# Kernel optimization log

Hardware: AMD Instinct MI355X
Metric: run time of the kernel (lower is better)

The kernel has to match this reference:

```python
import jax, jax.numpy as jnp
import numpy as np

B, T, F, H, V = 4096, 128, 256, 64, 32
EMB = 8
IN = EMB + 1  # 8-dim feature embedding + 1 Y_past channel
EPS = 1e-3    # keras LayerNorm/BatchNorm default epsilon


def lstm(x, Wk, Wr, b, h0, c0):
    """Keras-convention LSTM (gate order i,f,g,o). x: [B,T,D] -> ([B,T,H], h, c)."""
    def step(carry, xt):
        h, c = carry
        z = xt @ Wk + h @ Wr + b
        i, f, g, o = jnp.split(z, 4, axis=-1)
        c = jax.nn.sigmoid(f) * c + jax.nn.sigmoid(i) * jnp.tanh(g)
        h = jax.nn.sigmoid(o) * jnp.tanh(c)
        return (h, c), h
    (h, c), hs = jax.lax.scan(step, (h0, c0), jnp.swapaxes(x, 0, 1))
    return jnp.swapaxes(hs, 0, 1), h, c


def setup_inputs() -> dict:
    key = jax.random.key(0)
    ks = iter(jax.random.split(key, 32))
    n = lambda *s: jax.random.normal(next(ks), s, jnp.float32) * 0.05
    return {
        "X": jax.random.normal(next(ks), (B, T, F), jnp.float32),
        "Y_past": jax.random.randint(next(ks), (B, T), 0, V),
        "ln_gamma": jnp.ones((F,), jnp.float32), "ln_beta": jnp.zeros((F,), jnp.float32),
        "W1": n(F, 32), "b1": jnp.zeros((32,), jnp.float32),
        "bn_gamma": jnp.ones((32,), jnp.float32), "bn_beta": jnp.zeros((32,), jnp.float32),
        "bn_mean": jnp.zeros((32,), jnp.float32), "bn_var": jnp.ones((32,), jnp.float32),
        "W2": n(32, 16), "b2": jnp.zeros((16,), jnp.float32),
        "W3": n(16, EMB), "b3": jnp.zeros((EMB,), jnp.float32),
        "enc_fk": n(IN, 4 * H), "enc_fr": n(H, 4 * H), "enc_fb": jnp.zeros((4 * H,), jnp.float32),
        "enc_bk": n(IN, 4 * H), "enc_br": n(H, 4 * H), "enc_bb": jnp.zeros((4 * H,), jnp.float32),
        "Wsh": n(2 * H, H), "bsh": jnp.zeros((H,), jnp.float32),
        "Wsc": n(2 * H, H), "bsc": jnp.zeros((H,), jnp.float32),
        "Wq": n(H, 2 * H), "bq": jnp.zeros((2 * H,), jnp.float32),
        "dec_k": n(2 * H, 4 * H), "dec_r": n(H, 4 * H), "dec_b": jnp.zeros((4 * H,), jnp.float32),
        "Wo": n(H, V), "bo": jnp.zeros((V,), jnp.float32),
    }


def reference(X, Y_past, ln_gamma, ln_beta, W1, b1, bn_gamma, bn_beta, bn_mean, bn_var,
              W2, b2, W3, b3, enc_fk, enc_fr, enc_fb, enc_bk, enc_br, enc_bb,
              Wsh, bsh, Wsc, bsc, Wq, bq, dec_k, dec_r, dec_b, Wo, bo):
    b = X.shape[0]
    # LayerNorm over feature axis
    mu = jnp.mean(X, axis=-1, keepdims=True)
    var = jnp.var(X, axis=-1, keepdims=True)
    xn = (X - mu) * jax.lax.rsqrt(var + EPS) * ln_gamma + ln_beta
    # feature MLP (dropout inactive at inference); BatchNorm in inference mode
    e = jax.nn.relu(xn @ W1 + b1)
    e = (e - bn_mean) * jax.lax.rsqrt(bn_var + EPS) * bn_gamma + bn_beta
    e = jax.nn.relu(e @ W2 + b2)
    e = jax.nn.relu(e @ W3 + b3)
    seq = jnp.concatenate([e, Y_past.astype(jnp.float32)[..., None]], axis=-1)  # [B,T,9]
    # Bidirectional LSTM encoder (merge_mode='concat')
    h0 = jnp.zeros((b, H), seq.dtype)
    c0 = jnp.zeros((b, H), seq.dtype)
    fwd_out, fh, fc = lstm(seq, enc_fk, enc_fr, enc_fb, h0, c0)
    bwd_out, bh, bc = lstm(seq[:, ::-1], enc_bk, enc_br, enc_bb, h0, c0)
    enc = jnp.concatenate([fwd_out, bwd_out[:, ::-1]], axis=-1)  # [B,T,2H]
    # state projections and query
    sh = jnp.concatenate([fh, bh], axis=-1) @ Wsh + bsh  # [B,H]
    sc = jnp.concatenate([fc, bc], axis=-1) @ Wsc + bsc  # [B,H]
    q = (sh @ Wq + bq)[:, None, :]                       # [B,1,2H]
    # keras Attention: dot-product scores, softmax over keys
    scores = jnp.einsum('bqd,btd->bqt', q, enc)
    w = jax.nn.softmax(scores, axis=-1)
    att = jnp.einsum('bqt,btd->bqd', w, enc)             # [B,1,2H]
    # decoder LSTM (length-1 sequence) with projected initial state
    dec_out, _, _ = lstm(att, dec_k, dec_r, dec_b, sh, sc)  # [B,1,H]
    return jax.nn.softmax(dec_out @ Wo + bo, axis=-1)       # [B,1,V]
```

## Files before the change

### kernel.cpp

```cpp
#include <hip/hip_runtime.h>
#include <math.h>

#define BB 4096
#define TT 128
#define FF 256
#define VV 32
#define LN_EPS 1e-3f

typedef __attribute__((ext_vector_type(8))) short short8;
typedef __attribute__((ext_vector_type(4))) float f32x4;

template <int M> struct IC { static constexpr int value = M; };

__device__ __forceinline__ float sigm(float x) {
    return __builtin_amdgcn_rcpf(1.0f + __builtin_amdgcn_exp2f(-1.442695041f * x));
}
__device__ __forceinline__ float tanhfast(float x) {
    float e = __builtin_amdgcn_exp2f(2.885390082f * x);
    return 1.0f - 2.0f * __builtin_amdgcn_rcpf(e + 1.0f);
}
__device__ __forceinline__ unsigned short f2bf(float f) {
    union { float f; unsigned u; } v; v.f = f;
    unsigned r = v.u + 0x7FFFu + ((v.u >> 16) & 1u);
    return (unsigned short)(r >> 16);
}
__device__ __forceinline__ float bf2f(unsigned short h) {
    union { unsigned u; float f; } v; v.u = ((unsigned)h) << 16; return v.f;
}

__global__ __launch_bounds__(256, 3) void k_mlp2(
    const float* __restrict__ X, const int* __restrict__ Yp,
    const float* __restrict__ lng, const float* __restrict__ lnb,
    const float* __restrict__ W1, const float* __restrict__ b1,
    const float* __restrict__ bng, const float* __restrict__ bnb,
    const float* __restrict__ bnm, const float* __restrict__ bnv,
    const float* __restrict__ W2, const float* __restrict__ b2,
    const float* __restrict__ W3, const float* __restrict__ b3,
    unsigned int* __restrict__ sqpk, unsigned short* __restrict__ yv)
{
    __shared__ unsigned short w1fh[8192], w1fl[8192];
    __shared__ unsigned short w2fh[512], w2fl[512];
    __shared__ unsigned short w3fh[512], w3fl[512];
    __shared__ float bD1[32], bnSs[32], bnBs[32], b2s[16], b3s[8];
    __shared__ float e1s[4][16][33];
    __shared__ float e2s[4][16][17];

    const int tid = threadIdx.x;
    for (int e = tid; e < 8192; e += 256) {
        int j = e & 7, lane = (e >> 3) & 63, nt = (e >> 9) & 1, ks = e >> 10;
        int c = ks * 32 + (lane >> 4) * 8 + j;
        int n = nt * 16 + (lane & 15);
        float v = lng[c] * W1[c * 32 + n];
        unsigned short hi = f2bf(v);
        w1fh[e] = hi; w1fl[e] = f2bf(v - bf2f(hi));
    }
    for (int e = tid; e < 512; e += 256) {
        int j = e & 7, lane = e >> 3;
        int k = (lane >> 4) * 8 + j, n = lane & 15;
        float v2 = W2[k * 16 + n];
        unsigned short h2 = f2bf(v2);
        w2fh[e] = h2; w2fl[e] = f2bf(v2 - bf2f(h2));
        float v3 = (k < 16 && n < 8) ? W3[k * 8 + n] : 0.f;
        unsigned short h3 = f2bf(v3);
        w3fh[e] = h3; w3fl[e] = f2bf(v3 - bf2f(h3));
    }
    if (tid < 32) {
        float a = b1[tid];
        for (int c2 = 0; c2 < 256; ++c2) a += lnb[c2] * W1[c2 * 32 + tid];
        bD1[tid] = a;
        float sc = bng[tid] * rsqrtf(bnv[tid] + LN_EPS);
        bnSs[tid] = sc; bnBs[tid] = bnb[tid] - bnm[tid] * sc;
    } else if (tid < 48) b2s[tid - 32] = b2[tid - 32];
    else if (tid < 56) b3s[tid - 48] = b3[tid - 48];
    __syncthreads();

    const int wv = tid >> 6, l = tid & 63;
    const int r = l & 15, q = l >> 4;
    const int ntiles = (BB * TT) / 16;
    for (int tile = blockIdx.x * 4 + wv; tile < ntiles; tile += gridDim.x * 4) {
        const size_t rowbase = (size_t)tile * 16;
        const float* xrow = X + (rowbase + r) * FF + q * 8;
        float xd[64];
        #pragma unroll
        for (int ks = 0; ks < 8; ++ks) {
            float4 p0 = *(const float4*)(xrow + ks * 32);
            float4 p1 = *(const float4*)(xrow + ks * 32 + 4);
            xd[ks * 8 + 0] = p0.x; xd[ks * 8 + 1] = p0.y; xd[ks * 8 + 2] = p0.z; xd[ks * 8 + 3] = p0.w;
            xd[ks * 8 + 4] = p1.x; xd[ks * 8 + 5] = p1.y; xd[ks * 8 + 6] = p1.z; xd[ks * 8 + 7] = p1.w;
        }
        float s = 0.f, ss = 0.f;
        #pragma unroll
        for (int i = 0; i < 64; ++i) { s += xd[i]; ss += xd[i] * xd[i]; }
        s += __shfl_xor(s, 16);  s += __shfl_xor(s, 32);
        ss += __shfl_xor(ss, 16); ss += __shfl_xor(ss, 32);
        float mu = s * (1.0f / FF);
        float var = ss * (1.0f / FF) - mu * mu;
        float rs = rsqrtf(var + LN_EPS);

        f32x4 acc0 = {bD1[r], bD1[r], bD1[r], bD1[r]};
        f32x4 acc1 = {bD1[16 + r], bD1[16 + r], bD1[16 + r], bD1[16 + r]};
        #pragma unroll
        for (int ks = 0; ks < 8; ++ks) {
            short8 ah, al;
            #pragma unroll
            for (int j = 0; j < 8; ++j) {
                float xn = (xd[ks * 8 + j] - mu) * rs;
                unsigned short hi = f2bf(xn);
                ah[j] = (short)hi; al[j] = (short)f2bf(xn - bf2f(hi));
            }
            short8 bh0 = *(const short8*)&w1fh[((ks * 2 + 0) * 64 + l) * 8];
            short8 bl0 = *(const short8*)&w1fl[((ks * 2 + 0) * 64 + l) * 8];
            short8 bh1 = *(const short8*)&w1fh[((ks * 2 + 1) * 64 + l) * 8];
            short8 bl1 = *(const short8*)&w1fl[((ks * 2 + 1) * 64 + l) * 8];
            acc0 = __builtin_amdgcn_mfma_f32_16x16x32_bf16(ah, bh0, acc0, 0, 0, 0);
            acc0 = __builtin_amdgcn_mfma_f32_16x16x32_bf16(al, bh0, acc0, 0, 0, 0);
            acc0 = __builtin_amdgcn_mfma_f32_16x16x32_bf16(ah, bl0, acc0, 0, 0, 0);
            acc1 = __builtin_amdgcn_mfma_f32_16x16x32_bf16(ah, bh1, acc1, 0, 0, 0);
            acc1 = __builtin_amdgcn_mfma_f32_16x16x32_bf16(al, bh1, acc1, 0, 0, 0);
            acc1 = __builtin_amdgcn_mfma_f32_16x16x32_bf16(ah, bl1, acc1, 0, 0, 0);
        }
        #pragma unroll
        for (int i = 0; i < 4; ++i) {
            int row = q * 4 + i;
            float z0 = fmaxf(acc0[i], 0.f) * bnSs[r] + bnBs[r];
            float z1 = fmaxf(acc1[i], 0.f) * bnSs[16 + r] + bnBs[16 + r];
            e1s[wv][row][r] = z0;
            e1s[wv][row][16 + r] = z1;
        }
        __builtin_amdgcn_wave_barrier();

        short8 a2h, a2l;
        #pragma unroll
        for (int j = 0; j < 8; ++j) {
            float v = e1s[wv][r][q * 8 + j];
            unsigned short hi = f2bf(v);
            a2h[j] = (short)hi; a2l[j] = (short)f2bf(v - bf2f(hi));
        }
        f32x4 acc2 = {b2s[r], b2s[r], b2s[r], b2s[r]};
        {
            short8 bh = *(const short8*)&w2fh[l * 8];
            short8 bl = *(const short8*)&w2fl[l * 8];
            acc2 = __builtin_amdgcn_mfma_f32_16x16x32_bf16(a2h, bh, acc2, 0, 0, 0);
            acc2 = __builtin_amdgcn_mfma_f32_16x16x32_bf16(a2l, bh, acc2, 0, 0, 0);
            acc2 = __builtin_amdgcn_mfma_f32_16x16x32_bf16(a2h, bl, acc2, 0, 0, 0);
        }
        #pragma unroll
        for (int i = 0; i < 4; ++i) e2s[wv][q * 4 + i][r] = fmaxf(acc2[i], 0.f);
        __builtin_amdgcn_wave_barrier();

        short8 a3h = (short8){0,0,0,0,0,0,0,0}, a3l = (short8){0,0,0,0,0,0,0,0};
        if (q < 2) {
            #pragma unroll
            for (int j = 0; j < 8; ++j) {
                float v = e2s[wv][r][q * 8 + j];
                unsigned short hi = f2bf(v);
                a3h[j] = (short)hi; a3l[j] = (short)f2bf(v - bf2f(hi));
            }
        }
        float b3v = (r < 8) ? b3s[r] : 0.f;
        f32x4 acc3 = {b3v, b3v, b3v, b3v};
        {
            short8 bh = *(const short8*)&w3fh[l * 8];
            short8 bl = *(const short8*)&w3fl[l * 8];
            acc3 = __builtin_amdgcn_mfma_f32_16x16x32_bf16(a3h, bh, acc3, 0, 0, 0);
            acc3 = __builtin_amdgcn_mfma_f32_16x16x32_bf16(a3l, bh, acc3, 0, 0, 0);
            acc3 = __builtin_amdgcn_mfma_f32_16x16x32_bf16(a3h, bl, acc3, 0, 0, 0);
        }
        if (r < 8) {
            #pragma unroll
            for (int i = 0; i < 4; ++i) {
                size_t grow = rowbase + q * 4 + i;
                float e3 = fmaxf(acc3[i], 0.f);
                unsigned short bfh = f2bf(e3);
                unsigned short bfe = f2bf(e3 - bf2f(bfh));
                unsigned int wself = ((unsigned)bfh << 16) | (unsigned)bfe;
                unsigned int wnbr = __shfl_xor(wself, 1);
                unsigned int outw = (r & 1) ? ((wself << 16) | (wnbr & 0xFFFFu))
                                            : ((wnbr & 0xFFFF0000u) | (wself >> 16));
                sqpk[grow * 8 + (r >> 1) + ((r & 1) ? 4 : 0)] = outw;
            }
        } else if (r == 8) {
            #pragma unroll
            for (int i = 0; i < 4; ++i) {
                size_t grow = rowbase + q * 4 + i;
                yv[grow] = f2bf((float)Yp[grow]);
            }
        }
        __builtin_amdgcn_wave_barrier();
    }
}

#define R1_SEQ 0u
#define R1_YV  65536u
#define R1_HP  69632u
#define R1_SZ  87040u

__global__ __launch_bounds__(512, 1) void k_rnn1(
    const unsigned int* __restrict__ g_sqpk, const unsigned short* __restrict__ g_yv,
    const float* __restrict__ fk, const float* __restrict__ fr, const float* __restrict__ fb,
    const float* __restrict__ bk, const float* __restrict__ br, const float* __restrict__ bbv,
    unsigned int* __restrict__ enc,
    float* __restrict__ hfin, float* __restrict__ cfin,
    int s0)
{
    __shared__ __align__(16) unsigned char arena[R1_SZ];
    unsigned int*  seqU   = (unsigned int*)(arena + R1_SEQ);
    unsigned short* yvS   = (unsigned short*)(arena + R1_YV);
    unsigned int*  hpackU = (unsigned int*)(arena + R1_HP);

    const int tid = threadIdx.x;
    const int sbase = s0 + blockIdx.x * 16;
    const int wv = tid >> 6, l = tid & 63;
    const int d = wv >> 2, w = wv & 3;
    const int r = l & 15, q = l >> 4;
    const int u = (w << 4) + r;

    for (int i = tid; i < 16 * TT * 8; i += 512) {
        int smp = i >> 10;
        int rem = i & 1023;
        int t = rem >> 3, j = rem & 7;
        unsigned int v = g_sqpk[(size_t)(sbase + smp) * (TT * 8) + rem];
        seqU[((t * 2 + (j >> 2)) * 16 + smp) * 4 + (j & 3)] = v;
    }
    for (int i = tid; i < 16 * TT; i += 512) {
        int smp = i >> 7, t = i & 127;
        yvS[t * 16 + smp] = g_yv[(size_t)(sbase + smp) * TT + t];
    }

    const float* Wr = d ? br : fr;
    const float* Wk = d ? bk : fk;
    const float* Bz = d ? bbv : fb;
    short8 Bh[3][4], Bl[3][4];
    float bz[4];
    #pragma unroll
    for (int g = 0; g < 4; ++g) {
        int col = (g << 6) + u;
        bz[g] = Bz[col];
        #pragma unroll
        for (int kt = 0; kt < 3; ++kt) {
            #pragma unroll
            for (int j = 0; j < 8; ++j) {
                int kg = kt * 32 + q * 8 + j;
                float v = (kg < 64) ? Wr[kg * 256 + col]
                        : (kg < 73) ? Wk[(kg - 64) * 256 + col] : 0.f;
                unsigned short hi = f2bf(v);
                Bh[kt][g][j] = (short)hi;
                Bl[kt][g][j] = (short)f2bf(v - bf2f(hi));
            }
        }
    }

    const unsigned int* hrd0 = hpackU + (d * 16 + r) * 68 + q * 4;
    const unsigned int* hrd1 = hrd0 + 2176;
    const int wofs = w * 8 + (r >> 1) + ((r & 1) ? 32 : 0);
    const int elb = ((blockIdx.x * 16 + q * 4) * TT) * 64 + d * 32 + (u >> 1);

    for (int i = tid; i < 4352; i += 512) hpackU[i] = 0u;
    float c4[4] = {0.f, 0.f, 0.f, 0.f};
    __syncthreads();

    for (int t = 0; t < TT; ++t) {
        const int ts = d ? (TT - 1 - t) : t;
        const int buf = t & 1;
        const unsigned int* hp = buf ? hrd1 : hrd0;
        short8 A0h = *(const short8*)(hp);
        short8 A1h = *(const short8*)(hp + 16);
        short8 A0l = *(const short8*)(hp + 32);
        short8 A1l = *(const short8*)(hp + 48);
        short8 A2h = (short8){0,0,0,0,0,0,0,0};
        short8 A2l = (short8){0,0,0,0,0,0,0,0};
        if (q == 0) {
            const unsigned int* sp = seqU + (ts * 32 + r) * 4;
            A2h = *(const short8*)sp;
            A2l = *(const short8*)(sp + 64);
        } else if (q == 1) {
            A2h[0] = (short)yvS[ts * 16 + r];
        }
        f32x4 z[4];
        #pragma unroll
        for (int g = 0; g < 4; ++g) {
            f32x4 acc = {bz[g], bz[g], bz[g], bz[g]};
            acc = __builtin_amdgcn_mfma_f32_16x16x32_bf16(A0h, Bh[0][g], acc, 0, 0, 0);
            acc = __builtin_amdgcn_mfma_f32_16x16x32_bf16(A0l, Bh[0][g], acc, 0, 0, 0);
            acc = __builtin_amdgcn_mfma_f32_16x16x32_bf16(A0h, Bl[0][g], acc, 0, 0, 0);
            acc = __builtin_amdgcn_mfma_f32_16x16x32_bf16(A1h, Bh[1][g], acc, 0, 0, 0);
            acc = __builtin_amdgcn_mfma_f32_16x16x32_bf16(A1l, Bh[1][g], acc, 0, 0, 0);
            acc = __builtin_amdgcn_mfma_f32_16x16x32_bf16(A1h, Bl[1][g], acc, 0, 0, 0);
            acc = __builtin_amdgcn_mfma_f32_16x16x32_bf16(A2h, Bh[2][g], acc, 0, 0, 0);
            acc = __builtin_amdgcn_mfma_f32_16x16x32_bf16(A2l, Bh[2][g], acc, 0, 0, 0);
            acc = __builtin_amdgcn_mfma_f32_16x16x32_bf16(A2h, Bl[2][g], acc, 0, 0, 0);
            z[g] = acc;
        }
        const int nbase = ((buf ^ 1) * 2 + d) * 16;
        #pragma unroll
        for (int i = 0; i < 4; ++i) {
            float zi = z[0][i], zf = z[1][i], zg = z[2][i], zo = z[3][i];
            float cc = sigm(zf) * c4[i] + sigm(zi) * tanhfast(zg);
            float hh = sigm(zo) * tanhfast(cc);
            c4[i] = cc;
            int smp = (q << 2) + i;
            unsigned short bfh = f2bf(hh);
            unsigned short bfe = f2bf(hh - bf2f(bfh));
            unsigned int wself = ((unsigned)bfh << 16) | (unsigned)bfe;
            unsigned int wnbr = __shfl_xor(wself, 1);
            unsigned int outw = (r & 1) ? ((wself << 16) | (wnbr & 0xFFFFu))
                                        : ((wnbr & 0xFFFF0000u) | (wself >> 16));
            hpackU[(nbase + smp) * 68 + wofs] = outw;
            if ((r & 1) == 0) enc[elb + i * (TT * 64) + ts * 64] = outw;
            if (t == TT - 1) {
                hfin[(size_t)(sbase + smp) * 128 + (d << 6) + u] = hh;
                cfin[(size_t)(sbase + smp) * 128 + (d << 6) + u] = cc;
            }
        }
        __syncthreads();
    }
}

__global__ __launch_bounds__(256, 4) void k_att(
    const unsigned short* __restrict__ enc,
    const float* __restrict__ hfin, const float* __restrict__ cfin,
    const float* __restrict__ Wsh, const float* __restrict__ bsh,
    const float* __restrict__ Wsc, const float* __restrict__ bsc,
    const float* __restrict__ Wq,  const float* __restrict__ bq,
    const float* __restrict__ dk,  const float* __restrict__ dr, const float* __restrict__ dbv,
    const float* __restrict__ Wo,  const float* __restrict__ bo,
    float* __restrict__ out, int s0)
{
    __shared__ unsigned short el[TT][136];
    __shared__ float st[128], ct[128], shS[64], scS[64], qS[128], pS[128], attS[128], zdS[256], hdS[64], red[8];

    int tid = threadIdx.x;
    int bloc = blockIdx.x;
    int s = s0 + bloc;

    for (int i = tid; i < TT * 16; i += 256) {
        int t = i >> 4, c = i & 15;
        *(short8*)&el[t][c * 8] = *(const short8*)&enc[(size_t)bloc * TT * 128 + t * 128 + c * 8];
    }
    if (tid < 128) { st[tid] = hfin[(size_t)s * 128 + tid]; ct[tid] = cfin[(size_t)s * 128 + tid]; }
    __syncthreads();

    if (tid < 128) {
        int uu = tid & 63;
        const float* Wm = (tid < 64) ? Wsh : Wsc;
        const float* sv = (tid < 64) ? st : ct;
        float a = (tid < 64) ? bsh[uu] : bsc[uu];
        #pragma unroll 4
        for (int j = 0; j < 128; ++j) a += sv[j] * Wm[j * 64 + uu];
        if (tid < 64) shS[uu] = a; else scS[uu] = a;
    }
    __syncthreads();
    if (tid < 128) {
        float a = bq[tid];
        #pragma unroll 4
        for (int uu = 0; uu < 64; ++uu) a += shS[uu] * Wq[uu * 128 + tid];
        qS[tid] = a;
    }
    __syncthreads();
    float sc_val = 0.f;
    int wvv = tid >> 6, lnn = tid & 63;
    if (tid < 128) {
        float a = 0.f;
        #pragma unroll 2
        for (int c = 0; c < 16; ++c) {
            short8 e8 = *(const short8*)&el[tid][c * 8];
            #pragma unroll
            for (int j2 = 0; j2 < 8; ++j2) a += qS[c * 8 + j2] * bf2f((unsigned short)e8[j2]);
        }
        sc_val = a;
        float m = a;
        #pragma unroll
        for (int mk = 1; mk < 64; mk <<= 1) m = fmaxf(m, __shfl_xor(m, mk));
        if (lnn == 0) red[wvv] = m;
    }
    __syncthreads();
    float gmax = fmaxf(red[0], red[1]);
    if (tid < 128) {
        float ev = expf(sc_val - gmax);
        pS[tid] = ev;
        float s2 = ev;
        #pragma unroll
        for (int mk = 1; mk < 64; mk <<= 1) s2 += __shfl_xor(s2, mk);
        if (lnn == 0) red[4 + wvv] = s2;
    }
    __syncthreads();
    float denom = red[4] + red[5];
    if (tid < 128) {
        float a = 0.f;
        #pragma unroll 4
        for (int t2 = 0; t2 < TT; ++t2) a += pS[t2] * bf2f(el[t2][tid]);
        attS[tid] = a / denom;
    }
    __syncthreads();
    if (tid < 256) {
        float a = dbv[tid];
        #pragma unroll 4
        for (int j = 0; j < 128; ++j) a += attS[j] * dk[j * 256 + tid];
        #pragma unroll 4
        for (int j = 0; j < 64; ++j)  a += shS[j] * dr[j * 256 + tid];
        zdS[tid] = a;
    }
    __syncthreads();
    if (tid < 64) {
        float zi = zdS[tid], zf = zdS[64 + tid], zg = zdS[128 + tid], zo = zdS[192 + tid];
        float cc = sigm(zf) * scS[tid] + sigm(zi) * tanhfast(zg);
        hdS[tid] = sigm(zo) * tanhfast(cc);
    }
    __syncthreads();
    if (tid < 32) {
        float a = bo[tid];
        #pragma unroll
        for (int uu = 0; uu < 64; ++uu) a += hdS[uu] * Wo[uu * 32 + tid];
        float m = a;
        #pragma unroll
        for (int mk = 1; mk < 32; mk <<= 1) m = fmaxf(m, __shfl_xor(m, mk));
        float e = expf(a - m);
        float s2 = e;
        #pragma unroll
        for (int mk = 1; mk < 32; mk <<= 1) s2 += __shfl_xor(s2, mk);
        out[(size_t)s * VV + tid] = e / s2;
    }
}

#define A_SEQ   0u
#define A_YV    65536u
#define A_HP    69632u
#define A_SGRID 87040u
#define A_SH    103424u
#define A_SC    107520u
#define A_Q     111616u
#define A_ATT   119808u
#define A_L     128000u
#define A_SZ    128064u

__global__ __launch_bounds__(512, 1) void k_rnn(
    const unsigned int* __restrict__ g_sqpk, const unsigned short* __restrict__ g_yv,
    const float* __restrict__ fk, const float* __restrict__ fr, const float* __restrict__ fb,
    const float* __restrict__ bk, const float* __restrict__ br, const float* __restrict__ bbv,
    const float* __restrict__ Wsh, const float* __restrict__ bsh,
    const float* __restrict__ Wsc, const float* __restrict__ bsc,
    const float* __restrict__ Wq,  const float* __restrict__ bq,
    const float* __restrict__ dk,  const float* __restrict__ dr, const float* __restrict__ db,
    const float* __restrict__ Wo,  const float* __restrict__ bo,
    float* __restrict__ out)
{
    __shared__ __align__(16) unsigned char arena[A_SZ];
    unsigned int*  seqU  = (unsigned int*)(arena + A_SEQ);
    unsigned short* yvS  = (unsigned short*)(arena + A_YV);
    unsigned int*  hpackU = (unsigned int*)(arena + A_HP);
    float* sgridF = (float*)(arena + A_SGRID);
    float* hfinL  = (float*)(arena + A_SGRID);
    float* cfinL  = hfinL + 2048;
    float* zdS    = (float*)(arena + A_SGRID);
    float* shS    = (float*)(arena + A_SH);
    float* scS    = (float*)(arena + A_SC);
    float* qS     = (float*)(arena + A_Q);
    float* pT     = (float*)(arena + A_Q);
    float* attS   = (float*)(arena + A_ATT);
    float* hdS    = (float*)(arena + A_ATT);
    float* lS     = (float*)(arena + A_L);

    const int tid = threadIdx.x;
    const int sbase = blockIdx.x * 16;
    const int wv = tid >> 6, l = tid & 63;
    const int d = wv >> 2, w = wv & 3;
    const int r = l & 15, q = l >> 4;
    const int u = (w << 4) + r;

    for (int i = tid; i < 16 * TT * 8; i += 512) {
        int smp = i >> 10;
        int rem = i & 1023;
        int t = rem >> 3, j = rem & 7;
        unsigned int v = g_sqpk[(size_t)(sbase + smp) * (TT * 8) + rem];
        seqU[((t * 2 + (j >> 2)) * 16 + smp) * 4 + (j & 3)] = v;
    }
    for (int i = tid; i < 16 * TT; i += 512) {
        int smp = i >> 7, t = i & 127;
        yvS[t * 16 + smp] = g_yv[(size_t)(sbase + smp) * TT + t];
    }

    const float* Wr = d ? br : fr;
    const float* Wk = d ? bk : fk;
    const float* Bz = d ? bbv : fb;
    short8 Bh[3][4], Bl[3][4];
    float bz[4];
    #pragma unroll
    for (int g = 0; g < 4; ++g) {
        int col = (g << 6) + u;
        bz[g] = Bz[col];
        #pragma unroll
        for (int kt = 0; kt < 3; ++kt) {
            #pragma unroll
            for (int j = 0; j < 8; ++j) {
                int kg = kt * 32 + q * 8 + j;
                float v = (kg < 64) ? Wr[kg * 256 + col]
                        : (kg < 73) ? Wk[(kg - 64) * 256 + col] : 0.f;
                unsigned short hi = f2bf(v);
                Bh[kt][g][j] = (short)hi;
                Bl[kt][g][j] = (short)f2bf(v - bf2f(hi));
            }
        }
    }
    short8 Bq0h = (short8){0,0,0,0,0,0,0,0}, Bq1h = (short8){0,0,0,0,0,0,0,0};

    const unsigned int* hrd0 = hpackU + (d * 16 + r) * 68 + q * 4;
    const unsigned int* hrd1 = hrd0 + 2176;
    const int wofs = w * 8 + (r >> 1) + ((r & 1) ? 32 : 0);
    __syncthreads();

    auto run_phase = [&](auto mode_c) {
        constexpr int mode = decltype(mode_c)::value;
        for (int i = tid; i < 4352; i += 512) hpackU[i] = 0u;
        float c4[4] = {0.f, 0.f, 0.f, 0.f};
        float aacc[4] = {0.f, 0.f, 0.f, 0.f};
        __syncthreads();
        for (int t = 0; t < TT; ++t) {
            const int ts = d ? (TT - 1 - t) : t;
            const int buf = t & 1;
            const unsigned int* hp = buf ? hrd1 : hrd0;
            short8 A0h = *(const short8*)(hp);
            short8 A1h = *(const short8*)(hp + 16);
            short8 A0l = *(const short8*)(hp + 32);
            short8 A1l = *(const short8*)(hp + 48);
            short8 A2h = (short8){0,0,0,0,0,0,0,0};
            short8 A2l = (short8){0,0,0,0,0,0,0,0};
            if (q == 0) {
                const unsigned int* sp = seqU + (ts * 32 + r) * 4;
                A2h = *(const short8*)sp;
                A2l = *(const short8*)(sp + 64);
            } else if (q == 1) {
                A2h[0] = (short)yvS[ts * 16 + r];
            }
            if constexpr (mode == 1) {
                if (w == 0 && t > 0) {
                    f32x4 sa = {0.f, 0.f, 0.f, 0.f};
                    sa = __builtin_amdgcn_mfma_f32_16x16x32_bf16(A0h, Bq0h, sa, 0, 0, 0);
                    sa = __builtin_amdgcn_mfma_f32_16x16x32_bf16(A1h, Bq1h, sa, 0, 0, 0);
                    if (q == (r >> 2)) {
                        int tp = d ? (TT - t) : (t - 1);
                        sgridF[(d * 16 + r) * 128 + tp] = sa[r & 3];
                    }
                }
            }
            f32x4 z[4];
            #pragma unroll
            for (int g = 0; g < 4; ++g) {
                f32x4 acc = {bz[g], bz[g], bz[g], bz[g]};
                acc = __builtin_amdgcn_mfma_f32_16x16x32_bf16(A0h, Bh[0][g], acc, 0, 0, 0);
                acc = __builtin_amdgcn_mfma_f32_16x16x32_bf16(A0l, Bh[0][g], acc, 0, 0, 0);
                acc = __builtin_amdgcn_mfma_f32_16x16x32_bf16(A0h, Bl[0][g], acc, 0, 0, 0);
                acc = __builtin_amdgcn_mfma_f32_16x16x32_bf16(A1h, Bh[1][g], acc, 0, 0, 0);
                acc = __builtin_amdgcn_mfma_f32_16x16x32_bf16(A1l, Bh[1][g], acc, 0, 0, 0);
                acc = __builtin_amdgcn_mfma_f32_16x16x32_bf16(A1h, Bl[1][g], acc, 0, 0, 0);
                acc = __builtin_amdgcn_mfma_f32_16x16x32_bf16(A2h, Bh[2][g], acc, 0, 0, 0);
                acc = __builtin_amdgcn_mfma_f32_16x16x32_bf16(A2l, Bh[2][g], acc, 0, 0, 0);
                acc = __builtin_amdgcn_mfma_f32_16x16x32_bf16(A2h, Bl[2][g], acc, 0, 0, 0);
                z[g] = acc;
            }
            const int nbase = ((buf ^ 1) * 2 + d) * 16;
            #pragma unroll
            for (int i = 0; i < 4; ++i) {
                float zi = z[0][i], zf = z[1][i], zg = z[2][i], zo = z[3][i];
                float cc = sigm(zf) * c4[i] + sigm(zi) * tanhfast(zg);
                float hh = sigm(zo) * tanhfast(cc);
                c4[i] = cc;
                int smp = (q << 2) + i;
                unsigned short bfh = f2bf(hh);
                unsigned short bfe = f2bf(hh - bf2f(bfh));
                unsigned int wself = ((unsigned)bfh << 16) | (unsigned)bfe;
                unsigned int wnbr = __shfl_xor(wself, 1);
                unsigned int outw = (r & 1) ? ((wself << 16) | (wnbr & 0xFFFFu))
                                            : ((wnbr & 0xFFFF0000u) | (wself >> 16));
                hpackU[(nbase + smp) * 68 + wofs] = outw;
                if constexpr (mode == 2) aacc[i] += pT[ts * 16 + smp] * hh;
                if constexpr (mode == 0) {
                    if (t == TT - 1) {
                        hfinL[smp * 128 + (d << 6) + u] = hh;
                        cfinL[smp * 128 + (d << 6) + u] = cc;
                    }
                }
            }
            __syncthreads();
        }
        if constexpr (mode == 1) {
            if (w == 0) {
                short8 A0h = *(const short8*)(hrd0);
                short8 A1h = *(const short8*)(hrd0 + 16);
                f32x4 sa = {0.f, 0.f, 0.f, 0.f};
                sa = __builtin_amdgcn_mfma_f32_16x16x32_bf16(A0h, Bq0h, sa, 0, 0, 0);
                sa = __builtin_amdgcn_mfma_f32_16x16x32_bf16(A1h, Bq1h, sa, 0, 0, 0);
                if (q == (r >> 2)) {
                    int tp = d ? 0 : (TT - 1);
                    sgridF[(d * 16 + r) * 128 + tp] = sa[r & 3];
                }
            }
            __syncthreads();
        }
        if constexpr (mode == 2) {
            #pragma unroll
            for (int i = 0; i < 4; ++i) {
                int smp = (q << 2) + i;
                attS[smp * 128 + (d << 6) + u] = aacc[i] / lS[smp];
            }
            __syncthreads();
        }
    };

    run_phase(IC<0>{});
    for (int o = tid; o < 2048; o += 512) {
        int kind = o >> 10, smp = (o >> 6) & 15, uu = o & 63;
        const float* src = kind ? (cfinL + smp * 128) : (hfinL + smp * 128);
        const float* Wm = kind ? Wsc : Wsh;
        float a = kind ? bsc[uu] : bsh[uu];
        #pragma unroll 4
        for (int j = 0; j < 128; ++j) a += src[j] * Wm[j * 64 + uu];
        (kind ? scS : shS)[smp * 64 + uu] = a;
    }
    __syncthreads();
    for (int o = tid; o < 2048; o += 512) {
        int smp = o >> 7, dd = o & 127;
        float a = bq[dd];
        #pragma unroll 4
        for (int j = 0; j < 64; ++j) a += shS[smp * 64 + j] * Wq[j * 128 + dd];
        qS[smp * 128 + dd] = a;
    }
    __syncthreads();
    if (w == 0) {
        #pragma unroll
        for (int j = 0; j < 8; ++j) {
            Bq0h[j] = (short)f2bf(qS[r * 128 + (d << 6) + q * 8 + j]);
            Bq1h[j] = (short)f2bf(qS[r * 128 + (d << 6) + 32 + q * 8 + j]);
        }
    }
    __syncthreads();

    run_phase(IC<1>{});
    {
        int smp = tid >> 5, sl = tid & 31;
        float sv[4];
        #pragma unroll
        for (int p = 0; p < 4; ++p) {
            int t = sl + 32 * p;
            sv[p] = sgridF[smp * 128 + t] + sgridF[(16 + smp) * 128 + t];
        }
        float m = fmaxf(fmaxf(sv[0], sv[1]), fmaxf(sv[2], sv[3]));
        #pragma unroll
        for (int mk = 1; mk < 32; mk <<= 1) m = fmaxf(m, __shfl_xor(m, mk));
        float lsum = 0.f;
        #pragma unroll
        for (int p = 0; p < 4; ++p) lsum += __expf(sv[p] - m);
        #pragma unroll
        for (int mk = 1; mk < 32; mk <<= 1) lsum += __shfl_xor(lsum, mk);
        __syncthreads();
        #pragma unroll
        for (int p = 0; p < 4; ++p) pT[(sl + 32 * p) * 16 + smp] = __expf(sv[p] - m);
        if (sl == 0) lS[smp] = lsum;
    }
    __syncthreads();

    run_phase(IC<2>{});

    for (int o = tid; o < 4096; o += 512) {
        int smp = o >> 8, col = o & 255;
        float a = db[col];
        #pragma unroll 4
        for (int j = 0; j < 128; ++j) a += attS[smp * 128 + j] * dk[j * 256 + col];
        #pragma unroll 4
        for (int j = 0; j < 64; ++j)  a += shS[smp * 64 + j] * dr[j * 256 + col];
        zdS[smp * 256 + col] = a;
    }
    __syncthreads();
    for (int o = tid; o < 1024; o += 512) {
        int smp = o >> 6, uu = o & 63;
        float zi = zdS[smp * 256 + uu], zf = zdS[smp * 256 + 64 + uu];
        float zg = zdS[smp * 256 + 128 + uu], zo = zdS[smp * 256 + 192 + uu];
        float cc = sigm(zf) * scS[smp * 64 + uu] + sigm(zi) * tanhfast(zg);
        hdS[smp * 64 + uu] = sigm(zo) * tanhfast(cc);
    }
    __syncthreads();
    {
        int smp = tid >> 5, v = tid & 31;
        float a = bo[v];
        #pragma unroll 4
        for (int j = 0; j < 64; ++j) a += hdS[smp * 64 + j] * Wo[j * 32 + v];
        float m = a;
        #pragma unroll
        for (int mk = 1; mk < 32; mk <<= 1) m = fmaxf(m, __shfl_xor(m, mk));
        float e = __expf(a - m);
        float s2 = e;
        #pragma unroll
        for (int mk = 1; mk < 32; mk <<= 1) s2 += __shfl_xor(s2, mk);
        out[(size_t)(sbase + smp) * VV + v] = e / s2;
    }
}

extern "C" void kernel_launch(void* const* d_in, const int* in_sizes, int n_in,
                              void* d_out, int out_size, void* d_ws, size_t ws_size,
                              hipStream_t stream) {
    const float* X   = (const float*)d_in[0];
    const int*   Yp  = (const int*)d_in[1];
    const float* lng = (const float*)d_in[2];
    const float* lnb = (const float*)d_in[3];
    const float* W1  = (const float*)d_in[4];
    const float* b1  = (const float*)d_in[5];
    const float* bng = (const float*)d_in[6];
    const float* bnb = (const float*)d_in[7];
    const float* bnm = (const float*)d_in[8];
    const float* bnv = (const float*)d_in[9];
    const float* W2  = (const float*)d_in[10];
    const float* b2  = (const float*)d_in[11];
    const float* W3  = (const float*)d_in[12];
    const float* b3  = (const float*)d_in[13];
    const float* fk  = (const float*)d_in[14];
    const float* fr  = (const float*)d_in[15];
    const float* fb  = (const float*)d_in[16];
    const float* bk  = (const float*)d_in[17];
    const float* br  = (const float*)d_in[18];
    const float* bbv = (const float*)d_in[19];
    const float* Wsh = (const float*)d_in[20];
    const float* bsh = (const float*)d_in[21];
    const float* Wsc = (const float*)d_in[22];
    const float* bsc = (const float*)d_in[23];
    const float* Wq  = (const float*)d_in[24];
    const float* bq  = (const float*)d_in[25];
    const float* dk  = (const float*)d_in[26];
    const float* dr  = (const float*)d_in[27];
    const float* db  = (const float*)d_in[28];
    const float* Wo  = (const float*)d_in[29];
    const float* bo  = (const float*)d_in[30];

    unsigned int*   sqpk = (unsigned int*)d_ws;
    unsigned short* yv   = (unsigned short*)(sqpk + (size_t)BB * TT * 8);
    float*          hfin = (float*)(yv + (size_t)BB * TT);
    float*          cfin = hfin + (size_t)BB * 128;
    unsigned int*   encp = (unsigned int*)(cfin + (size_t)BB * 128);
    const size_t baseB = (size_t)((char*)encp - (char*)d_ws);

    int nch = 0;
    if (ws_size >= baseB + (size_t)BB * TT * 128 * 2)            nch = 1;
    else if (ws_size >= baseB + (size_t)(BB / 2) * TT * 128 * 2) nch = 2;

    k_mlp2<<<768, 256, 0, stream>>>(X, Yp, lng, lnb, W1, b1, bng, bnb, bnm, bnv,
                                    W2, b2, W3, b3, sqpk, yv);
    if (nch) {
        const int cs = BB / nch;
        for (int c = 0; c < nch; ++c) {
            int s0 = c * cs;
            k_rnn1<<<cs / 16, 512, 0, stream>>>(sqpk, yv, fk, fr, fb, bk, br, bbv,
                                                encp, hfin, cfin, s0);
            k_att<<<cs, 256, 0, stream>>>((const unsigned short*)encp, hfin, cfin,
                                          Wsh, bsh, Wsc, bsc, Wq, bq,
                                          dk, dr, db, Wo, bo, (float*)d_out, s0);
        }
    } else {
        k_rnn<<<BB / 16, 512, 0, stream>>>(sqpk, yv, fk, fr, fb, bk, br, bbv,
                                           Wsh, bsh, Wsc, bsc, Wq, bq, dk, dr, db, Wo, bo,
                                           (float*)d_out);
    }
}
```

Measured before the change: 504.7 us.

## Store embedding sequence as single bf16 and drop its low-part MFMA

The MLP embedding output is now stored as plain bf16 rather than a hi/lo bf16 pair. This halves the packed sequence buffer and the shared-memory arena, and removes one MFMA per gate per timestep in the recurrent loop. The shared-memory sequence layout is changed to a padded stride of 68 words, and more chunk counts (4 and 8) are allowed when the workspace is small. In exchange, the encoder input loses about 8 bits of mantissa precision, which may slightly perturb accuracy.

```diff
diff --git a/kernel.cpp b/kernel.cpp
--- a/kernel.cpp
+++ b/kernel.cpp
@@ -171,13 +171,9 @@
             for (int i = 0; i < 4; ++i) {
                 size_t grow = rowbase + q * 4 + i;
                 float e3 = fmaxf(acc3[i], 0.f);
-                unsigned short bfh = f2bf(e3);
-                unsigned short bfe = f2bf(e3 - bf2f(bfh));
-                unsigned int wself = ((unsigned)bfh << 16) | (unsigned)bfe;
+                unsigned int wself = (unsigned)f2bf(e3);
                 unsigned int wnbr = __shfl_xor(wself, 1);
-                unsigned int outw = (r & 1) ? ((wself << 16) | (wnbr & 0xFFFFu))
-                                            : ((wnbr & 0xFFFF0000u) | (wself >> 16));
-                sqpk[grow * 8 + (r >> 1) + ((r & 1) ? 4 : 0)] = outw;
+                if ((r & 1) == 0) sqpk[grow * 4 + (r >> 1)] = (wnbr << 16) | wself;
             }
         } else if (r == 8) {
             #pragma unroll
@@ -191,9 +187,9 @@
 }
 
 #define R1_SEQ 0u
-#define R1_YV  65536u
-#define R1_HP  69632u
-#define R1_SZ  87040u
+#define R1_YV  34816u
+#define R1_HP  38912u
+#define R1_SZ  56320u
 
 __global__ __launch_bounds__(512, 1) void k_rnn1(
     const unsigned int* __restrict__ g_sqpk, const unsigned short* __restrict__ g_yv,
@@ -204,9 +200,9 @@
     int s0)
 {
     __shared__ __align__(16) unsigned char arena[R1_SZ];
-    unsigned int*  seqU   = (unsigned int*)(arena + R1_SEQ);
-    unsigned short* yvS   = (unsigned short*)(arena + R1_YV);
-    unsigned int*  hpackU = (unsigned int*)(arena + R1_HP);
+    unsigned int*   seqU   = (unsigned int*)(arena + R1_SEQ);
+    unsigned short* yvS    = (unsigned short*)(arena + R1_YV);
+    unsigned int*   hpackU = (unsigned int*)(arena + R1_HP);
 
     const int tid = threadIdx.x;
     const int sbase = s0 + blockIdx.x * 16;
@@ -215,12 +211,10 @@
     const int r = l & 15, q = l >> 4;
     const int u = (w << 4) + r;
 
-    for (int i = tid; i < 16 * TT * 8; i += 512) {
-        int smp = i >> 10;
-        int rem = i & 1023;
-        int t = rem >> 3, j = rem & 7;
-        unsigned int v = g_sqpk[(size_t)(sbase + smp) * (TT * 8) + rem];
-        seqU[((t * 2 + (j >> 2)) * 16 + smp) * 4 + (j & 3)] = v;
+    for (int i = tid; i < 16 * TT * 4; i += 512) {
+        int smp = i >> 9, rem = i & 511;
+        int t = rem >> 2, j = rem & 3;
+        seqU[t * 68 + smp * 4 + j] = g_sqpk[(size_t)(sbase + smp) * (TT * 4) + rem];
     }
     for (int i = tid; i < 16 * TT; i += 512) {
         int smp = i >> 7, t = i & 127;
@@ -268,11 +262,8 @@
         short8 A0l = *(const short8*)(hp + 32);
         short8 A1l = *(const short8*)(hp + 48);
         short8 A2h = (short8){0,0,0,0,0,0,0,0};
-        short8 A2l = (short8){0,0,0,0,0,0,0,0};
         if (q == 0) {
-            const unsigned int* sp = seqU + (ts * 32 + r) * 4;
-            A2h = *(const short8*)sp;
-            A2l = *(const short8*)(sp + 64);
+            A2h = *(const short8*)(seqU + ts * 68 + r * 4);
         } else if (q == 1) {
             A2h[0] = (short)yvS[ts * 16 + r];
         }
@@ -287,7 +278,6 @@
             acc = __builtin_amdgcn_mfma_f32_16x16x32_bf16(A1l, Bh[1][g], acc, 0, 0, 0);
             acc = __builtin_amdgcn_mfma_f32_16x16x32_bf16(A1h, Bl[1][g], acc, 0, 0, 0);
             acc = __builtin_amdgcn_mfma_f32_16x16x32_bf16(A2h, Bh[2][g], acc, 0, 0, 0);
-            acc = __builtin_amdgcn_mfma_f32_16x16x32_bf16(A2l, Bh[2][g], acc, 0, 0, 0);
             acc = __builtin_amdgcn_mfma_f32_16x16x32_bf16(A2h, Bl[2][g], acc, 0, 0, 0);
             z[g] = acc;
         }
@@ -423,15 +413,15 @@
 }
 
 #define A_SEQ   0u
-#define A_YV    65536u
-#define A_HP    69632u
-#define A_SGRID 87040u
-#define A_SH    103424u
-#define A_SC    107520u
-#define A_Q     111616u
-#define A_ATT   119808u
-#define A_L     128000u
-#define A_SZ    128064u
+#define A_YV    34816u
+#define A_HP    38912u
+#define A_SGRID 56320u
+#define A_SH    72704u
+#define A_SC    76800u
+#define A_Q     80896u
+#define A_ATT   89088u
+#define A_L     97280u
+#define A_SZ    97344u
 
 __global__ __launch_bounds__(512, 1) void k_rnn(
     const unsigned int* __restrict__ g_sqpk, const unsigned short* __restrict__ g_yv,
@@ -445,9 +435,9 @@
     float* __restrict__ out)
 {
     __shared__ __align__(16) unsigned char arena[A_SZ];
-    unsigned int*  seqU  = (unsigned int*)(arena + A_SEQ);
-    unsigned short* yvS  = (unsigned short*)(arena + A_YV);
-    unsigned int*  hpackU = (unsigned int*)(arena + A_HP);
+    unsigned int*   seqU   = (unsigned int*)(arena + A_SEQ);
+    unsigned short* yvS    = (unsigned short*)(arena + A_YV);
+    unsigned int*   hpackU = (unsigned int*)(arena + A_HP);
     float* sgridF = (float*)(arena + A_SGRID);
     float* hfinL  = (float*)(arena + A_SGRID);
     float* cfinL  = hfinL + 2048;
@@ -467,12 +457,10 @@
     const int r = l & 15, q = l >> 4;
     const int u = (w << 4) + r;
 
-    for (int i = tid; i < 16 * TT * 8; i += 512) {
-        int smp = i >> 10;
-        int rem = i & 1023;
-        int t = rem >> 3, j = rem & 7;
-        unsigned int v = g_sqpk[(size_t)(sbase + smp) * (TT * 8) + rem];
-        seqU[((t * 2 + (j >> 2)) * 16 + smp) * 4 + (j & 3)] = v;
+    for (int i = tid; i < 16 * TT * 4; i += 512) {
+        int smp = i >> 9, rem = i & 511;
+        int t = rem >> 2, j = rem & 3;
+        seqU[t * 68 + smp * 4 + j] = g_sqpk[(size_t)(sbase + smp) * (TT * 4) + rem];
     }
     for (int i = tid; i < 16 * TT; i += 512) {
         int smp = i >> 7, t = i & 127;
@@ -523,11 +511,8 @@
             short8 A0l = *(const short8*)(hp + 32);
             short8 A1l = *(const short8*)(hp + 48);
             short8 A2h = (short8){0,0,0,0,0,0,0,0};
-            short8 A2l = (short8){0,0,0,0,0,0,0,0};
             if (q == 0) {
-                const unsigned int* sp = seqU + (ts * 32 + r) * 4;
-                A2h = *(const short8*)sp;
-                A2l = *(const short8*)(sp + 64);
+                A2h = *(const short8*)(seqU + ts * 68 + r * 4);
             } else if (q == 1) {
                 A2h[0] = (short)yvS[ts * 16 + r];
             }
@@ -553,7 +538,6 @@
                 acc = __builtin_amdgcn_mfma_f32_16x16x32_bf16(A1l, Bh[1][g], acc, 0, 0, 0);
                 acc = __builtin_amdgcn_mfma_f32_16x16x32_bf16(A1h, Bl[1][g], acc, 0, 0, 0);
                 acc = __builtin_amdgcn_mfma_f32_16x16x32_bf16(A2h, Bh[2][g], acc, 0, 0, 0);
-                acc = __builtin_amdgcn_mfma_f32_16x16x32_bf16(A2l, Bh[2][g], acc, 0, 0, 0);
                 acc = __builtin_amdgcn_mfma_f32_16x16x32_bf16(A2h, Bl[2][g], acc, 0, 0, 0);
                 z[g] = acc;
             }
@@ -730,15 +714,18 @@
     const float* bo  = (const float*)d_in[30];
 
     unsigned int*   sqpk = (unsigned int*)d_ws;
-    unsigned short* yv   = (unsigned short*)(sqpk + (size_t)BB * TT * 8);
+    unsigned short* yv   = (unsigned short*)(sqpk + (size_t)BB * TT * 4);
     float*          hfin = (float*)(yv + (size_t)BB * TT);
     float*          cfin = hfin + (size_t)BB * 128;
     unsigned int*   encp = (unsigned int*)(cfin + (size_t)BB * 128);
     const size_t baseB = (size_t)((char*)encp - (char*)d_ws);
+    const size_t encFull = (size_t)BB * TT * 128 * 2;
 
     int nch = 0;
-    if (ws_size >= baseB + (size_t)BB * TT * 128 * 2)            nch = 1;
-    else if (ws_size >= baseB + (size_t)(BB / 2) * TT * 128 * 2) nch = 2;
+    if      (ws_size >= baseB + encFull)     nch = 1;
+    else if (ws_size >= baseB + encFull / 2) nch = 2;
+    else if (ws_size >= baseB + encFull / 4) nch = 4;
+    else if (ws_size >= baseB + encFull / 8) nch = 8;
 
     k_mlp2<<<768, 256, 0, stream>>>(X, Yp, lng, lnb, W1, b1, bng, bnb, bnm, bnv,
                                     W2, b2, W3, b3, sqpk, yv);
```

Measured after the change: 490.4 us. 2.8% less time.
